# Optimization experiments

Hardware: AMD Instinct MI355X
Metric: run time of the kernel (lower is better)

## Reference

```python
import jax, jax.numpy as jnp
import numpy as np

LRELU_SLOPE = 0.1  # correlate_operator uses F.leaky_relu_(corr, 0.1)


def _conv2d(x, w, b):
    # x: [B,Ci,H,W], w: [Co,Ci,kh,kw], stride 1, padding SAME (=padding=1 for 3x3)
    y = jax.lax.conv_general_dilated(x, w, (1, 1), 'SAME',
                                     dimension_numbers=('NCHW', 'OIHW', 'NCHW'))
    return y + b[None, :, None, None]


def correlate(x1, x2):
    # spatial_correlation_sample(x1, x2, kernel_size=3, patch_size=1, stride=1,
    # padding=1): with patch_size=1 the only displacement is (0,0), so the cost
    # volume is a 3x3 window sum of the per-pixel channel dot product.
    # Then divided by C and leaky_relu(0.1) as in correlate_operator.
    prod = jnp.sum(x1 * x2, axis=1, keepdims=True)  # [B,1,H,W]
    box = jnp.ones((1, 1, 3, 3), prod.dtype)
    corr = jax.lax.conv_general_dilated(prod, box, (1, 1), 'SAME',
                                        dimension_numbers=('NCHW', 'OIHW', 'NCHW'))
    corr = corr / x1.shape[1]
    return jnp.where(corr > 0, corr, LRELU_SLOPE * corr)


def deform_conv2d(x, offset, w):
    # mmcv DeformConv2d: kernel 3x3, stride 1, pad 1, dilation 1, deform_groups=1,
    # bias=False. offset: [B, 2*kh*kw, H, W], per kernel tap k: (dy_k, dx_k).
    B, Cin, H, W = x.shape
    O, _, kh, kw = w.shape
    K = kh * kw
    off = offset.reshape(B, K, 2, H, W)
    dy, dx = off[:, :, 0], off[:, :, 1]  # [B,K,H,W]
    ky, kx = jnp.meshgrid(jnp.arange(kh), jnp.arange(kw), indexing='ij')
    # sampling position: p + p_k + offset_k (pad=1 cancels the kernel-center shift)
    y = jnp.arange(H, dtype=x.dtype)[None, None, :, None] \
        + (ky.reshape(-1) - kh // 2).astype(x.dtype)[None, :, None, None] + dy
    xx = jnp.arange(W, dtype=x.dtype)[None, None, None, :] \
        + (kx.reshape(-1) - kw // 2).astype(x.dtype)[None, :, None, None] + dx
    y0 = jnp.floor(y)
    x0 = jnp.floor(xx)
    wy = (y - y0)[:, None]   # [B,1,K,H,W]
    wx = (xx - x0)[:, None]
    y0i = y0.astype(jnp.int32)
    x0i = x0.astype(jnp.int32)
    xf = x.reshape(B, Cin, H * W)

    def gather(yi, xi):
        valid = (yi >= 0) & (yi < H) & (xi >= 0) & (xi < W)  # zero padding outside
        idx = jnp.clip(yi, 0, H - 1) * W + jnp.clip(xi, 0, W - 1)
        v = jnp.take_along_axis(xf, idx.reshape(B, 1, K * H * W), axis=2)
        return v.reshape(B, Cin, K, H, W) * valid.astype(x.dtype)[:, None]

    v00 = gather(y0i, x0i)
    v01 = gather(y0i, x0i + 1)
    v10 = gather(y0i + 1, x0i)
    v11 = gather(y0i + 1, x0i + 1)
    samp = (v00 * (1 - wy) * (1 - wx) + v01 * (1 - wy) * wx
            + v10 * wy * (1 - wx) + v11 * wy * wx)  # [B,Cin,K,H,W]
    return jnp.einsum('bckhw,ock->bohw', samp, w.reshape(O, Cin, K))


def setup_inputs() -> dict:
    key = jax.random.key(0)
    ks = jax.random.split(key, 10)
    B, C, H, W = 4, 256, 64, 64
    s = 0.02
    return {
        'x_ref': jax.random.normal(ks[0], (B, C, H, W), jnp.float32),
        'x_next': jax.random.normal(ks[1], (B, C, H, W), jnp.float32),
        'w1': jax.random.normal(ks[2], (256, 1, 3, 3), jnp.float32) * s,
        'b1': jax.random.normal(ks[3], (256,), jnp.float32) * s,
        'w2': jax.random.normal(ks[4], (256, 256, 3, 3), jnp.float32) * s,
        'b2': jax.random.normal(ks[5], (256,), jnp.float32) * s,
        'w3': jax.random.normal(ks[6], (18, 256, 3, 3), jnp.float32) * s,
        'b3': jax.random.normal(ks[7], (18,), jnp.float32) * s,
        'w_dcn': jax.random.normal(ks[8], (256, 256, 3, 3), jnp.float32) * s,
        'idx': 4,
    }


def reference(x_ref, x_next, w1, b1, w2, b2, w3, b3, w_dcn, idx):
    # idx=4 -> corr_patch_size=1 (consistent with conv1 in_channels)
    corr = correlate(x_next, x_ref)                      # [B,1,H,W]
    h = jax.nn.relu(_conv2d(corr, w1, b1))               # [B,256,H,W]
    h = jax.nn.relu(_conv2d(h, w2, b2))                  # [B,256,H,W]
    offset = jax.nn.relu(_conv2d(h, w3, b3))             # [B,18,H,W]
    x_ref_cal = jax.nn.relu(deform_conv2d(x_ref, offset, w_dcn))
    return 0.5 * (x_next + x_ref_cal)
```

## Files before the change

### kernel.cpp

```cpp
#include <hip/hip_runtime.h>

typedef __attribute__((ext_vector_type(8))) short short8v;
typedef __attribute__((ext_vector_type(4))) float f32x4;
typedef __attribute__((ext_vector_type(2))) float f32x2;
typedef __attribute__((ext_vector_type(4))) unsigned int u32x4;

constexpr int Bsz = 4;
constexpr int Hh = 64, Wwd = 64;
constexpr int HWp = Hh * Wwd;
constexpr int NPIX = Bsz * HWp;
constexpr int HH = 66;
constexpr int HPIX = HH * HH;
constexpr int Kdim = 2304;
constexpr int NSTEP = 36;

constexpr size_t B_H1H  = 0;
constexpr size_t HALO_BYTES = (size_t)Bsz * HPIX * 256 * 2;
constexpr size_t B_H2H  = B_H1H + HALO_BYTES;
constexpr size_t B_XTH  = B_H2H + HALO_BYTES;
constexpr size_t B_PROD = B_XTH + HALO_BYTES;
constexpr size_t B_OFFP = B_PROD + (size_t)NPIX * 4;
constexpr size_t B_WB2  = B_OFFP + (size_t)NPIX * 32 * 4;
constexpr size_t B_WBD  = B_WB2 + (size_t)256 * Kdim * 2;
constexpr size_t B_WB3  = B_WBD + (size_t)256 * Kdim * 2;

static __device__ __forceinline__ unsigned short f2bf(float f) {
    unsigned u = __builtin_bit_cast(unsigned, f);
    u += 0x7FFFu + ((u >> 16) & 1u);
    return (unsigned short)(u >> 16);
}
static __device__ __forceinline__ unsigned cvt_pk_bf16(float lo, float hi) {
    unsigned r;
    asm("v_cvt_pk_bf16_f32 %0, %1, %2" : "=v"(r) : "v"(lo), "v"(hi));
    return r;
}
static __device__ __forceinline__ f32x2 pk_mul(f32x2 a, f32x2 b) {
    f32x2 d;
    asm("v_pk_mul_f32 %0, %1, %2" : "=v"(d) : "v"(a), "v"(b));
    return d;
}
static __device__ __forceinline__ f32x2 pk_fma(f32x2 a, f32x2 b, f32x2 c) {
    f32x2 d;
    asm("v_pk_fma_f32 %0, %1, %2, %3" : "=v"(d) : "v"(a), "v"(b), "v"(c));
    return d;
}
static __device__ __forceinline__ f32x2 unpack2(unsigned u) {
    f32x2 v;
    v.x = __builtin_bit_cast(float, u << 16);
    v.y = __builtin_bit_cast(float, u & 0xFFFF0000u);
    return v;
}
static __device__ __forceinline__ void gload_lds16(const void* g, void* l) {
    __builtin_amdgcn_global_load_lds((const __attribute__((address_space(1))) unsigned int*)g,
                                     (__attribute__((address_space(3))) unsigned int*)l, 16, 0, 0);
}
static __device__ __forceinline__ int swz(int u) {
    return (((u & 7) ^ ((u >> 3) & 7)) << 3);
}

__global__ void k_zero_ring(unsigned short* h1h, unsigned short* h2h, unsigned short* xth,
                            float* prod) {
    int blk = blockIdx.x;
    if (blk >= 3120) {
        unsigned* p = (unsigned*)prod + (size_t)(blk - 3120) * 128 + threadIdx.x;
        *p = 0;
        return;
    }
    int img = blk / 260;
    int rp = blk - img * 260;
    int buf = img >> 2, b = img & 3;
    int y, x;
    if (rp < 66) { y = 0; x = rp; }
    else if (rp < 132) { y = 65; x = rp - 66; }
    else { int s2 = rp - 132; y = 1 + (s2 >> 1); x = (s2 & 1) * 65; }
    unsigned short* base = (buf == 0) ? h1h : (buf == 1) ? h2h : xth;
    unsigned* p = (unsigned*)(base + ((size_t)b * HPIX + y * HH + x) * 256);
    p[threadIdx.x] = 0;
}

__global__ void k_prodx(const float* __restrict__ xr, const float* __restrict__ xn,
                        unsigned short* __restrict__ xth, float* __restrict__ prod) {
    __shared__ float t[32][33];
    __shared__ float red[8][33];
    int b = blockIdx.z;
    int c0 = blockIdx.y * 32;
    int y = blockIdx.x >> 1, x0 = (blockIdx.x & 1) * 32;
    int tx = threadIdx.x, ty = threadIdx.y;
    float part = 0.f;
#pragma unroll
    for (int i = 0; i < 32; i += 8) {
        size_t idx = ((size_t)b * 256 + c0 + ty + i) * HWp + y * Wwd + x0 + tx;
        float vr = xr[idx];
        float vn = xn[idx];
        t[ty + i][tx] = vr;
        part = fmaf(vr, vn, part);
    }
    red[ty][tx] = part;
    __syncthreads();
#pragma unroll
    for (int i = 0; i < 32; i += 8)
        xth[((size_t)b * HPIX + (y + 1) * HH + (x0 + ty + i + 1)) * 256 + c0 + tx] =
            f2bf(t[tx][ty + i]);
    if (ty == 0) {
        float s = red[0][tx] + red[1][tx] + red[2][tx] + red[3][tx] +
                  red[4][tx] + red[5][tx] + red[6][tx] + red[7][tx];
        atomicAdd(&prod[b * HWp + y * Wwd + x0 + tx], s);
    }
}

__global__ __launch_bounds__(256) void k_conv1c(const float* __restrict__ prod,
                                                const float* __restrict__ w1,
                                                const float* __restrict__ b1,
                                                unsigned short* __restrict__ h1h) {
    __shared__ float pp[5][36];
    __shared__ float pt[3][34];
    int px0 = blockIdx.x * 32;
    int b = px0 >> 12, y = (px0 & 4095) >> 6, x0 = px0 & 63;
    int tid = threadIdx.x;
    if (tid < 180) {
        int i = tid / 36, j = tid - i * 36;
        int yy = y - 2 + i, xx = x0 - 2 + j;
        float v = 0.f;
        if (yy >= 0 && yy < Hh && xx >= 0 && xx < Wwd) v = prod[b * HWp + yy * Wwd + xx];
        pp[i][j] = v;
    }
    __syncthreads();
    if (tid < 102) {
        int i = tid / 34, j = tid - i * 34;
        int yy = y - 1 + i, xx = x0 - 1 + j;
        float v = 0.f;
        if (yy >= 0 && yy < Hh && xx >= 0 && xx < Wwd) {
            float s = pp[i][j]     + pp[i][j + 1]     + pp[i][j + 2] +
                      pp[i + 1][j] + pp[i + 1][j + 1] + pp[i + 1][j + 2] +
                      pp[i + 2][j] + pp[i + 2][j + 1] + pp[i + 2][j + 2];
            s *= (1.0f / 256.0f);
            v = (s > 0.f) ? s : 0.1f * s;
        }
        pt[i][j] = v;
    }
    float wl[9];
#pragma unroll
    for (int k = 0; k < 9; ++k) wl[k] = w1[tid * 9 + k];
    float bias = b1[tid];
    __syncthreads();
    for (int p = 0; p < 32; ++p) {
        float acc = bias;
#pragma unroll
        for (int ky = 0; ky < 3; ++ky)
#pragma unroll
            for (int kx = 0; kx < 3; ++kx) acc = fmaf(pt[ky][p + kx], wl[ky * 3 + kx], acc);
        acc = fmaxf(acc, 0.f);
        h1h[((size_t)b * HPIX + (y + 1) * HH + (x0 + p + 1)) * 256 + tid] = f2bf(acc);
    }
}

__global__ void k_packall(const float* __restrict__ w2, const float* __restrict__ wd,
                          const float* __restrict__ w3,
                          unsigned short* __restrict__ wb2f, unsigned short* __restrict__ wbdf,
                          unsigned short* __restrict__ wb3) {
    int blk = blockIdx.x;
    if (blk < 4608) {
        const float* w = (blk < 2304) ? w2 : wd;
        unsigned short* out = (blk < 2304) ? wb2f : wbdf;
        int i = (blk % 2304) * 256 + threadIdx.x;
        int e = i & 7;
        int lane = (i >> 3) & 63;
        int mi = (i >> 9) & 1;
        int kf = (i >> 10) & 1;
        int rest = i >> 11;
        int s = rest % 36;
        int wv = rest / 36;
        int o = wv * 32 + mi * 16 + (lane & 15);
        int kk = s * 64 + (kf * 4 + (lane >> 4)) * 8 + e;
        int c = kk & 255, tap = kk >> 8;
        out[i] = f2bf(w[((size_t)o * 256 + c) * 9 + tap]);
    } else {
        int i = (blk - 4608) * 256 + threadIdx.x;
        int o = i / Kdim;
        int r = i - o * Kdim;
        int k = r >> 8, c = r & 255;
        float v = (o < 18) ? w3[((size_t)o * 256 + c) * 9 + k] : 0.f;
        wb3[i] = f2bf(v);
    }
}

__global__ __launch_bounds__(256) void k_conv2g(const unsigned short* __restrict__ h1h,
                                                const unsigned short* __restrict__ wbf,
                                                const float* __restrict__ bias,
                                                unsigned short* __restrict__ h2h) {
    __shared__ short S_s[4][64 * 64];
    const int tid = threadIdx.x;
    const int bid = blockIdx.x;
    const int lin = (bid & 7) * 64 + (bid >> 3);
    const int px0 = (lin >> 1) * 64;
    const int oblk = lin & 1;
    const int b = px0 >> 12;
    const unsigned short* hb = h1h + (size_t)b * HPIX * 256;
    const int pxl = tid >> 2;
    const int px = px0 + pxl;
    const int y = (px & 4095) >> 6, x = px & 63;
    const int u0 = (tid & 3) * 2;
    const int lane = tid & 63, wv = tid >> 6;
    const int ot = oblk * 4 + wv;
    const unsigned short* wfb = wbf + (size_t)ot * NSTEP * 2048 + lane * 8;
    const unsigned short* abase0 = hb + (size_t)((y + 1) * HH + (x + 1)) * 256 + u0 * 8;

    f32x4 acc[4][2] = {};
    u32x4 wA[2][4], wB[2][4];
    u32x4 aP[4], aQ[4];
    float bia[2];
#pragma unroll
    for (int oi = 0; oi < 2; ++oi) bia[oi] = bias[ot * 32 + oi * 16 + (lane & 15)];

    const int wr0 = pxl * 64 + ((u0 ^ (pxl & 7)) << 3);
    const int wr1 = pxl * 64 + (((u0 + 1) ^ (pxl & 7)) << 3);

    auto WLOAD = [&](int s, u32x4 (&wreg)[4]) {
#pragma unroll
        for (int f = 0; f < 4; ++f)
            wreg[f] = *(const u32x4*)(wfb + ((size_t)s * 4 + f) * 512);
    };
    auto ALOAD = [&](int s, u32x4& a0, u32x4& a1) {
        int tap = s >> 2, chunk = s & 3;
        int aoff = ((tap / 3 - 1) * HH + (tap % 3 - 1)) * 256 + chunk * 64;
        a0 = *(const u32x4*)(abase0 + aoff);
        a1 = *(const u32x4*)(abase0 + aoff + 8);
    };

    {
        u32x4 a0, a1, a2, a3;
        ALOAD(0, a0, a1);
        ALOAD(1, a2, a3);
        WLOAD(0, wA[0]);
        WLOAD(1, wA[1]);
        *(u32x4*)&S_s[0][wr0] = a0;
        *(u32x4*)&S_s[0][wr1] = a1;
        *(u32x4*)&S_s[1][wr0] = a2;
        *(u32x4*)&S_s[1][wr1] = a3;
        ALOAD(2, aP[0], aP[1]);
        ALOAD(3, aP[2], aP[3]);
        asm volatile("s_waitcnt lgkmcnt(0)" ::: "memory");
    }

    auto ITER2 = [&](int s, u32x4 (&wcur)[2][4], u32x4 (&wnxt)[2][4],
                     u32x4 (&aC)[4], u32x4 (&aN)[4], short* SBc, short* SBn) {
        __builtin_amdgcn_s_barrier();
        __builtin_amdgcn_sched_barrier(0);
        if (s + 2 < NSTEP) {
            *(u32x4*)&SBn[wr0] = aC[0];
            *(u32x4*)&SBn[wr1] = aC[1];
            *(u32x4*)&SBn[64 * 64 + wr0] = aC[2];
            *(u32x4*)&SBn[64 * 64 + wr1] = aC[3];
        }
        if (s + 4 < NSTEP) {
            ALOAD(s + 4, aN[0], aN[1]);
            ALOAD(s + 5, aN[2], aN[3]);
        }
        if (s + 2 < NSTEP) {
            WLOAD(s + 2, wnxt[0]);
            WLOAD(s + 3, wnxt[1]);
        }
#pragma unroll
        for (int half = 0; half < 2; ++half) {
            const short* SB = SBc + half * 64 * 64;
            short8v af[4][2];
#pragma unroll
            for (int pi = 0; pi < 4; ++pi) {
                int row = pi * 16 + (lane & 15);
#pragma unroll
                for (int kf = 0; kf < 2; ++kf) {
                    int c8 = kf * 4 + (lane >> 4);
                    af[pi][kf] = *(const short8v*)&SB[row * 64 + ((c8 ^ (row & 7)) << 3)];
                }
            }
            __builtin_amdgcn_s_setprio(1);
#pragma unroll
            for (int kf = 0; kf < 2; ++kf)
#pragma unroll
                for (int pi = 0; pi < 4; ++pi)
#pragma unroll
                    for (int oi = 0; oi < 2; ++oi)
                        acc[pi][oi] = __builtin_amdgcn_mfma_f32_16x16x32_bf16(
                            af[pi][kf], __builtin_bit_cast(short8v, wcur[half][kf * 2 + oi]),
                            acc[pi][oi], 0, 0, 0);
            __builtin_amdgcn_s_setprio(0);
        }
        asm volatile("s_waitcnt lgkmcnt(0)" ::: "memory");
    };

    for (int s4 = 0; s4 < NSTEP; s4 += 4) {
        ITER2(s4, wA, wB, aP, aQ, &S_s[0][0], &S_s[2][0]);
        ITER2(s4 + 2, wB, wA, aQ, aP, &S_s[2][0], &S_s[0][0]);
    }

#pragma unroll
    for (int pi = 0; pi < 4; ++pi) {
#pragma unroll
        for (int j = 0; j < 4; ++j) {
            int p2 = px0 + pi * 16 + (lane >> 4) * 4 + j;
            int yy = (p2 & 4095) >> 6, xx = p2 & 63;
            unsigned short* dst = h2h + ((size_t)b * HPIX + (yy + 1) * HH + (xx + 1)) * 256;
#pragma unroll
            for (int oi = 0; oi < 2; ++oi) {
                int o = ot * 32 + oi * 16 + (lane & 15);
                dst[o] = f2bf(fmaxf(acc[pi][oi][j] + bia[oi], 0.f));
            }
        }
    }
}

__global__ __launch_bounds__(256) void k_conv3g(const unsigned short* __restrict__ h2h,
                                                const unsigned short* __restrict__ wb,
                                                const float* __restrict__ bias,
                                                float* __restrict__ offp) {
    __shared__ short A_s[2][64 * 64];
    __shared__ short B_s[2][32 * 64];
    const int tid = threadIdx.x;
    const int px0 = blockIdx.x * 64;
    const int b = px0 >> 12;
    const unsigned short* hb = h2h + (size_t)b * HPIX * 256;

    const unsigned short* abase[2];
#pragma unroll
    for (int i = 0; i < 2; ++i) {
        int u = i * 256 + tid;
        int pxl = u >> 3;
        int pxg = px0 + pxl;
        int y = (pxg & 4095) >> 6, x = pxg & 63;
        abase[i] = hb + (size_t)((y + 1) * HH + (x + 1)) * 256 + swz(u);
    }
    const unsigned short* bbase = wb + (size_t)(tid >> 3) * Kdim + swz(tid);

    const int lane = tid & 63, wv = tid >> 6;
    f32x4 acc[2] = {};

    auto STAGE = [&](int s, int buf) {
        int tap = s >> 2, chunk = s & 3;
        int delta = ((tap / 3 - 1) * HH + (tap % 3 - 1)) * 256 + chunk * 64;
        short* Ab = &A_s[buf][0];
#pragma unroll
        for (int i = 0; i < 2; ++i) gload_lds16(abase[i] + delta, Ab + (i * 256 + tid) * 8);
        gload_lds16(bbase + s * 64, &B_s[buf][tid * 8]);
    };

    STAGE(0, 0);
    __syncthreads();
    for (int s = 0; s < NSTEP; ++s) {
        int cur = s & 1;
        if (s + 1 < NSTEP) STAGE(s + 1, cur ^ 1);
        const short* Ab = &A_s[cur][0];
        const short* Bb = &B_s[cur][0];
        short8v af[2], bf[2][2];
#pragma unroll
        for (int kf = 0; kf < 2; ++kf) {
            int row = wv * 16 + (lane & 15);
            int c8 = kf * 4 + (lane >> 4);
            af[kf] = *(const short8v*)&Ab[row * 64 + ((c8 ^ (row & 7)) << 3)];
        }
#pragma unroll
        for (int ni = 0; ni < 2; ++ni) {
            int row = ni * 16 + (lane & 15);
#pragma unroll
            for (int kf = 0; kf < 2; ++kf) {
                int c8 = kf * 4 + (lane >> 4);
                bf[ni][kf] = *(const short8v*)&B_s[cur][row * 64 + ((c8 ^ (row & 7)) << 3)];
            }
        }
#pragma unroll
        for (int kf = 0; kf < 2; ++kf)
#pragma unroll
            for (int ni = 0; ni < 2; ++ni)
                acc[ni] = __builtin_amdgcn_mfma_f32_16x16x32_bf16(af[kf], bf[ni][kf], acc[ni], 0, 0, 0);
        __syncthreads();
    }
#pragma unroll
    for (int j = 0; j < 4; ++j) {
        int px = px0 + wv * 16 + (lane >> 4) * 4 + j;
#pragma unroll
        for (int ni = 0; ni < 2; ++ni) {
            int o = ni * 16 + (lane & 15);
            float bv = (o < 18) ? bias[o] : 0.f;
            offp[(size_t)px * 32 + o] = fmaxf(acc[ni][j] + bv, 0.f);
        }
    }
}

__global__ __launch_bounds__(512) void k_dcng(const unsigned short* __restrict__ xth,
                                              const float* __restrict__ offp,
                                              const unsigned short* __restrict__ wbf,
                                              const float* __restrict__ xn,
                                              float* __restrict__ out) {
    __shared__ short S_s[4][64 * 64];
    const int tid = threadIdx.x;
    const int bid = blockIdx.x;
    const int px0 = ((bid & 7) * 32 + (bid >> 3)) * 64;
    const int b = px0 >> 12;
    const unsigned short* xb = xth + (size_t)b * HPIX * 256;
    const int pxl = tid >> 3;
    const int px = px0 + pxl;
    const int y = (px & 4095) >> 6, x = px & 63;
    const int u0 = tid & 7;
    const int lane = tid & 63, wv = tid >> 6;
    const unsigned short* wfb = wbf + (size_t)wv * NSTEP * 2048 + lane * 8;
    const float2* offv = (const float2*)offp;

    f32x4 acc[2][4] = {};
    u32x4 wA[2][4], wB[2][4];
    u32x4 g[2][4];
    const int wr0 = pxl * 64 + ((u0 ^ (pxl & 7)) << 3);

    const unsigned short* pcorner[4];
    f32x2 wpair[4];
    float2 offn;

    auto SETUP = [&](int tap, float dyo, float dxo) {
        int ky = tap / 3 - 1, kx = tap % 3 - 1;
        float ypos = (float)(y + ky) + dyo;
        float xpos = (float)(x + kx) + dxo;
        float y0f = floorf(ypos), x0f = floorf(xpos);
        float wy = ypos - y0f, wx = xpos - x0f;
        int y0 = (int)y0f, x0 = (int)x0f;
        bool y0v = (y0 >= 0) && (y0 < Hh), y1v = (y0 + 1 >= 0) && (y0 + 1 < Hh);
        bool x0v = (x0 >= 0) && (x0 < Wwd), x1v = (x0 + 1 >= 0) && (x0 + 1 < Wwd);
        int hy0 = min(max(y0, -1), 64) + 1, hy1 = min(max(y0 + 1, -1), 64) + 1;
        int hx0 = min(max(x0, -1), 64) + 1, hx1 = min(max(x0 + 1, -1), 64) + 1;
        float w0 = (1.f - wy) * (1.f - wx) * (float)(y0v && x0v);
        float w1 = (1.f - wy) * wx * (float)(y0v && x1v);
        float w2 = wy * (1.f - wx) * (float)(y1v && x0v);
        float w3 = wy * wx * (float)(y1v && x1v);
        wpair[0] = (f32x2){w0, w0};
        wpair[1] = (f32x2){w1, w1};
        wpair[2] = (f32x2){w2, w2};
        wpair[3] = (f32x2){w3, w3};
        pcorner[0] = xb + (size_t)((hy0 * HH + hx0) * 256) + u0 * 8;
        pcorner[1] = xb + (size_t)((hy0 * HH + hx1) * 256) + u0 * 8;
        pcorner[2] = xb + (size_t)((hy1 * HH + hx0) * 256) + u0 * 8;
        pcorner[3] = xb + (size_t)((hy1 * HH + hx1) * 256) + u0 * 8;
    };
    auto WLOAD = [&](int s, u32x4 (&wreg)[4]) {
#pragma unroll
        for (int f = 0; f < 4; ++f)
            wreg[f] = *(const u32x4*)(wfb + ((size_t)s * 4 + f) * 512);
    };
    auto GISSUE = [&](int s, u32x4 (&gr)[4]) {
        const int nco = (s & 3) * 64;
#pragma unroll
        for (int c = 0; c < 4; ++c) gr[c] = *(const u32x4*)(pcorner[c] + nco);
    };
    auto COMBINE_WRITE = [&](u32x4 (&gr)[4], short* SBn) {
        u32x4 res;
#pragma unroll
        for (int qd = 0; qd < 4; ++qd) {
            f32x2 a = pk_mul(unpack2(gr[0][qd]), wpair[0]);
            a = pk_fma(unpack2(gr[1][qd]), wpair[1], a);
            a = pk_fma(unpack2(gr[2][qd]), wpair[2], a);
            a = pk_fma(unpack2(gr[3][qd]), wpair[3], a);
            res[qd] = cvt_pk_bf16(a.x, a.y);
        }
        *(u32x4*)&SBn[wr0] = res;
    };

    {
        float2 o0 = offv[(size_t)px * 16];
        SETUP(0, o0.x, o0.y);
        u32x4 g0[4], g1[4];
        GISSUE(0, g0);
        GISSUE(1, g1);
        WLOAD(0, wA[0]);
        WLOAD(1, wA[1]);
        COMBINE_WRITE(g0, &S_s[0][0]);
        COMBINE_WRITE(g1, &S_s[1][0]);
        GISSUE(2, g[0]);
        GISSUE(3, g[1]);
        offn = offv[(size_t)px * 16 + 1];
        asm volatile("s_waitcnt lgkmcnt(0)" ::: "memory");
    }

    auto ITER2 = [&](int s, u32x4 (&wcur)[2][4], u32x4 (&wnxt)[2][4], short* SBc, short* SBn) {
        __builtin_amdgcn_s_barrier();
        __builtin_amdgcn_sched_barrier(0);
        if (s + 2 < NSTEP) {
            COMBINE_WRITE(g[0], SBn);
            COMBINE_WRITE(g[1], SBn + 64 * 64);
        }
        if ((s & 3) == 0 && s + 4 < NSTEP)
            SETUP((s + 4) >> 2, offn.x, offn.y);
        if ((s & 3) == 2 && ((s + 8) >> 2) < 9)
            offn = offv[(size_t)px * 16 + ((s + 8) >> 2)];
        if (s + 4 < NSTEP) {
            GISSUE(s + 4, g[0]);
            GISSUE(s + 5, g[1]);
        }
        if (s + 2 < NSTEP) {
            WLOAD(s + 2, wnxt[0]);
            WLOAD(s + 3, wnxt[1]);
        }
#pragma unroll
        for (int half = 0; half < 2; ++half) {
            const short* SB = SBc + half * 64 * 64;
            short8v sf[4][2];
#pragma unroll
            for (int ni = 0; ni < 4; ++ni) {
                int row = ni * 16 + (lane & 15);
#pragma unroll
                for (int kf = 0; kf < 2; ++kf) {
                    int c8 = kf * 4 + (lane >> 4);
                    sf[ni][kf] = *(const short8v*)&SB[row * 64 + ((c8 ^ (row & 7)) << 3)];
                }
            }
            __builtin_amdgcn_s_setprio(1);
#pragma unroll
            for (int kf = 0; kf < 2; ++kf)
#pragma unroll
                for (int mi = 0; mi < 2; ++mi)
#pragma unroll
                    for (int ni = 0; ni < 4; ++ni)
                        acc[mi][ni] = __builtin_amdgcn_mfma_f32_16x16x32_bf16(
                            __builtin_bit_cast(short8v, wcur[half][kf * 2 + mi]), sf[ni][kf],
                            acc[mi][ni], 0, 0, 0);
            __builtin_amdgcn_s_setprio(0);
        }
        asm volatile("s_waitcnt lgkmcnt(0)" ::: "memory");
    };

    for (int s4 = 0; s4 < NSTEP; s4 += 4) {
        ITER2(s4, wA, wB, &S_s[0][0], &S_s[2][0]);
        ITER2(s4 + 2, wB, wA, &S_s[2][0], &S_s[0][0]);
    }

#pragma unroll
    for (int mi = 0; mi < 2; ++mi) {
        int o = wv * 32 + mi * 16 + (lane >> 4) * 4;
#pragma unroll
        for (int j = 0; j < 4; ++j) {
            size_t rowbase = ((size_t)b * 256 + o + j) * HWp;
#pragma unroll
            for (int ni = 0; ni < 4; ++ni) {
                int p2 = (px0 + ni * 16 + (lane & 15)) & 4095;
                size_t idx = rowbase + p2;
                out[idx] = 0.5f * (xn[idx] + fmaxf(acc[mi][ni][j], 0.f));
            }
        }
    }
}

extern "C" void kernel_launch(void* const* d_in, const int* in_sizes, int n_in,
                              void* d_out, int out_size, void* d_ws, size_t ws_size,
                              hipStream_t stream) {
    const float* x_ref  = (const float*)d_in[0];
    const float* x_next = (const float*)d_in[1];
    const float* w1 = (const float*)d_in[2];
    const float* b1 = (const float*)d_in[3];
    const float* w2 = (const float*)d_in[4];
    const float* b2 = (const float*)d_in[5];
    const float* w3 = (const float*)d_in[6];
    const float* b3 = (const float*)d_in[7];
    const float* wd = (const float*)d_in[8];
    float* out = (float*)d_out;
    char* ws = (char*)d_ws;

    unsigned short* h1h = (unsigned short*)(ws + B_H1H);
    unsigned short* h2h = (unsigned short*)(ws + B_H2H);
    unsigned short* xth = (unsigned short*)(ws + B_XTH);
    float* prod = (float*)(ws + B_PROD);
    float* offp = (float*)(ws + B_OFFP);
    unsigned short* wb2f = (unsigned short*)(ws + B_WB2);
    unsigned short* wbdf = (unsigned short*)(ws + B_WBD);
    unsigned short* wb3  = (unsigned short*)(ws + B_WB3);

    k_zero_ring<<<3120 + 128, 128, 0, stream>>>(h1h, h2h, xth, prod);
    k_prodx<<<dim3(128, 8, Bsz), dim3(32, 8), 0, stream>>>(x_ref, x_next, xth, prod);
    k_packall<<<4896, 256, 0, stream>>>(w2, wd, w3, wb2f, wbdf, wb3);
    k_conv1c<<<NPIX / 32, 256, 0, stream>>>(prod, w1, b1, h1h);
    k_conv2g<<<512, 256, 0, stream>>>(h1h, wb2f, b2, h2h);
    k_conv3g<<<256, 256, 0, stream>>>(h2h, wb3, b3, offp);
    k_dcng<<<256, 512, 0, stream>>>(xth, offp, wbdf, x_next, out);
}
```

Measured before the change: 107.5 us.

## Restructure conv3 GEMM with register-held prepacked weights and deeper pipelining

The conv3 (256->18 offset) kernel stops staging A and B through global_load_lds. It now loads activations into registers, writes them to a swizzled 4-buffer LDS ring two steps ahead, and reads weights straight into registers from a new MFMA-fragment-packed layout produced by k_packall. Blocks are remapped across images in the same way as conv2/dcn, and the loop is unrolled two steps per barrier with setprio around the MFMAs. The aim is to hide load latency and cut LDS traffic and barriers, at the cost of more registers and more complex scheduling.

```diff
diff --git a/kernel.cpp b/kernel.cpp
--- a/kernel.cpp
+++ b/kernel.cpp
@@ -49,10 +49,6 @@
     v.x = __builtin_bit_cast(float, u << 16);
     v.y = __builtin_bit_cast(float, u & 0xFFFF0000u);
     return v;
-}
-static __device__ __forceinline__ void gload_lds16(const void* g, void* l) {
-    __builtin_amdgcn_global_load_lds((const __attribute__((address_space(1))) unsigned int*)g,
-                                     (__attribute__((address_space(3))) unsigned int*)l, 16, 0, 0);
 }
 static __device__ __forceinline__ int swz(int u) {
     return (((u & 7) ^ ((u >> 3) & 7)) << 3);
@@ -157,7 +153,7 @@
 __global__ void k_packall(const float* __restrict__ w2, const float* __restrict__ wd,
                           const float* __restrict__ w3,
                           unsigned short* __restrict__ wb2f, unsigned short* __restrict__ wbdf,
-                          unsigned short* __restrict__ wb3) {
+                          unsigned short* __restrict__ wb3f) {
     int blk = blockIdx.x;
     if (blk < 4608) {
         const float* w = (blk < 2304) ? w2 : wd;
@@ -176,11 +172,16 @@
         out[i] = f2bf(w[((size_t)o * 256 + c) * 9 + tap]);
     } else {
         int i = (blk - 4608) * 256 + threadIdx.x;
-        int o = i / Kdim;
-        int r = i - o * Kdim;
-        int k = r >> 8, c = r & 255;
-        float v = (o < 18) ? w3[((size_t)o * 256 + c) * 9 + k] : 0.f;
-        wb3[i] = f2bf(v);
+        int e = i & 7;
+        int lane = (i >> 3) & 63;
+        int oi = (i >> 9) & 1;
+        int kf = (i >> 10) & 1;
+        int s = i >> 11;
+        int o = oi * 16 + (lane & 15);
+        int kk = s * 64 + (kf * 4 + (lane >> 4)) * 8 + e;
+        int c = kk & 255, tap = kk >> 8;
+        float v = (o < 18) ? w3[((size_t)o * 256 + c) * 9 + tap] : 0.f;
+        wb3f[i] = f2bf(v);
     }
 }
 
@@ -310,77 +311,116 @@
 }
 
 __global__ __launch_bounds__(256) void k_conv3g(const unsigned short* __restrict__ h2h,
-                                                const unsigned short* __restrict__ wb,
+                                                const unsigned short* __restrict__ wb3f,
                                                 const float* __restrict__ bias,
                                                 float* __restrict__ offp) {
-    __shared__ short A_s[2][64 * 64];
-    __shared__ short B_s[2][32 * 64];
+    __shared__ short S_s[4][64 * 64];
     const int tid = threadIdx.x;
-    const int px0 = blockIdx.x * 64;
+    const int bid = blockIdx.x;
+    const int px0 = ((bid & 7) * 32 + (bid >> 3)) * 64;
     const int b = px0 >> 12;
     const unsigned short* hb = h2h + (size_t)b * HPIX * 256;
-
-    const unsigned short* abase[2];
-#pragma unroll
-    for (int i = 0; i < 2; ++i) {
-        int u = i * 256 + tid;
-        int pxl = u >> 3;
-        int pxg = px0 + pxl;
-        int y = (pxg & 4095) >> 6, x = pxg & 63;
-        abase[i] = hb + (size_t)((y + 1) * HH + (x + 1)) * 256 + swz(u);
-    }
-    const unsigned short* bbase = wb + (size_t)(tid >> 3) * Kdim + swz(tid);
-
+    const int pxl = tid >> 2;
+    const int px = px0 + pxl;
+    const int y = (px & 4095) >> 6, x = px & 63;
+    const int u0 = (tid & 3) * 2;
     const int lane = tid & 63, wv = tid >> 6;
+    const unsigned short* wfb = wb3f + lane * 8;
+    const unsigned short* abase0 = hb + (size_t)((y + 1) * HH + (x + 1)) * 256 + u0 * 8;
+
     f32x4 acc[2] = {};
-
-    auto STAGE = [&](int s, int buf) {
+    u32x4 wA[2][4], wB[2][4];
+    u32x4 aP[4], aQ[4];
+    float bia[2];
+#pragma unroll
+    for (int oi = 0; oi < 2; ++oi) {
+        int o = oi * 16 + (lane & 15);
+        bia[oi] = (o < 18) ? bias[o] : 0.f;
+    }
+
+    const int wr0 = pxl * 64 + ((u0 ^ (pxl & 7)) << 3);
+    const int wr1 = pxl * 64 + (((u0 + 1) ^ (pxl & 7)) << 3);
+
+    auto WLOAD = [&](int s, u32x4 (&wreg)[4]) {
+#pragma unroll
+        for (int f = 0; f < 4; ++f)
+            wreg[f] = *(const u32x4*)(wfb + ((size_t)s * 4 + f) * 512);
+    };
+    auto ALOAD = [&](int s, u32x4& a0, u32x4& a1) {
         int tap = s >> 2, chunk = s & 3;
-        int delta = ((tap / 3 - 1) * HH + (tap % 3 - 1)) * 256 + chunk * 64;
-        short* Ab = &A_s[buf][0];
-#pragma unroll
-        for (int i = 0; i < 2; ++i) gload_lds16(abase[i] + delta, Ab + (i * 256 + tid) * 8);
-        gload_lds16(bbase + s * 64, &B_s[buf][tid * 8]);
-    };
-
-    STAGE(0, 0);
-    __syncthreads();
-    for (int s = 0; s < NSTEP; ++s) {
-        int cur = s & 1;
-        if (s + 1 < NSTEP) STAGE(s + 1, cur ^ 1);
-        const short* Ab = &A_s[cur][0];
-        const short* Bb = &B_s[cur][0];
-        short8v af[2], bf[2][2];
-#pragma unroll
-        for (int kf = 0; kf < 2; ++kf) {
-            int row = wv * 16 + (lane & 15);
-            int c8 = kf * 4 + (lane >> 4);
-            af[kf] = *(const short8v*)&Ab[row * 64 + ((c8 ^ (row & 7)) << 3)];
-        }
-#pragma unroll
-        for (int ni = 0; ni < 2; ++ni) {
-            int row = ni * 16 + (lane & 15);
+        int aoff = ((tap / 3 - 1) * HH + (tap % 3 - 1)) * 256 + chunk * 64;
+        a0 = *(const u32x4*)(abase0 + aoff);
+        a1 = *(const u32x4*)(abase0 + aoff + 8);
+    };
+
+    {
+        u32x4 a0, a1, a2, a3;
+        ALOAD(0, a0, a1);
+        ALOAD(1, a2, a3);
+        WLOAD(0, wA[0]);
+        WLOAD(1, wA[1]);
+        *(u32x4*)&S_s[0][wr0] = a0;
+        *(u32x4*)&S_s[0][wr1] = a1;
+        *(u32x4*)&S_s[1][wr0] = a2;
+        *(u32x4*)&S_s[1][wr1] = a3;
+        ALOAD(2, aP[0], aP[1]);
+        ALOAD(3, aP[2], aP[3]);
+        asm volatile("s_waitcnt lgkmcnt(0)" ::: "memory");
+    }
+
+    auto ITER2 = [&](int s, u32x4 (&wcur)[2][4], u32x4 (&wnxt)[2][4],
+                     u32x4 (&aC)[4], u32x4 (&aN)[4], short* SBc, short* SBn) {
+        __builtin_amdgcn_s_barrier();
+        __builtin_amdgcn_sched_barrier(0);
+        if (s + 2 < NSTEP) {
+            *(u32x4*)&SBn[wr0] = aC[0];
+            *(u32x4*)&SBn[wr1] = aC[1];
+            *(u32x4*)&SBn[64 * 64 + wr0] = aC[2];
+            *(u32x4*)&SBn[64 * 64 + wr1] = aC[3];
+        }
+        if (s + 4 < NSTEP) {
+            ALOAD(s + 4, aN[0], aN[1]);
+            ALOAD(s + 5, aN[2], aN[3]);
+        }
+        if (s + 2 < NSTEP) {
+            WLOAD(s + 2, wnxt[0]);
+            WLOAD(s + 3, wnxt[1]);
+        }
+#pragma unroll
+        for (int half = 0; half < 2; ++half) {
+            const short* SB = SBc + half * 64 * 64;
+            short8v af[2];
 #pragma unroll
             for (int kf = 0; kf < 2; ++kf) {
+                int row = wv * 16 + (lane & 15);
                 int c8 = kf * 4 + (lane >> 4);
-                bf[ni][kf] = *(const short8v*)&B_s[cur][row * 64 + ((c8 ^ (row & 7)) << 3)];
+                af[kf] = *(const short8v*)&SB[row * 64 + ((c8 ^ (row & 7)) << 3)];
             }
-        }
-#pragma unroll
-        for (int kf = 0; kf < 2; ++kf)
-#pragma unroll
-            for (int ni = 0; ni < 2; ++ni)
-                acc[ni] = __builtin_amdgcn_mfma_f32_16x16x32_bf16(af[kf], bf[ni][kf], acc[ni], 0, 0, 0);
-        __syncthreads();
-    }
+            __builtin_amdgcn_s_setprio(1);
+#pragma unroll
+            for (int kf = 0; kf < 2; ++kf)
+#pragma unroll
+                for (int oi = 0; oi < 2; ++oi)
+                    acc[oi] = __builtin_amdgcn_mfma_f32_16x16x32_bf16(
+                        af[kf], __builtin_bit_cast(short8v, wcur[half][kf * 2 + oi]),
+                        acc[oi], 0, 0, 0);
+            __builtin_amdgcn_s_setprio(0);
+        }
+        asm volatile("s_waitcnt lgkmcnt(0)" ::: "memory");
+    };
+
+    for (int s4 = 0; s4 < NSTEP; s4 += 4) {
+        ITER2(s4, wA, wB, aP, aQ, &S_s[0][0], &S_s[2][0]);
+        ITER2(s4 + 2, wB, wA, aQ, aP, &S_s[2][0], &S_s[0][0]);
+    }
+
 #pragma unroll
     for (int j = 0; j < 4; ++j) {
-        int px = px0 + wv * 16 + (lane >> 4) * 4 + j;
-#pragma unroll
-        for (int ni = 0; ni < 2; ++ni) {
-            int o = ni * 16 + (lane & 15);
-            float bv = (o < 18) ? bias[o] : 0.f;
-            offp[(size_t)px * 32 + o] = fmaxf(acc[ni][j] + bv, 0.f);
+        int p2 = px0 + wv * 16 + (lane >> 4) * 4 + j;
+#pragma unroll
+        for (int oi = 0; oi < 2; ++oi) {
+            int o = oi * 16 + (lane & 15);
+            offp[(size_t)p2 * 32 + o] = fmaxf(acc[oi][j] + bia[oi], 0.f);
         }
     }
 }
@@ -566,13 +606,13 @@
     float* offp = (float*)(ws + B_OFFP);
     unsigned short* wb2f = (unsigned short*)(ws + B_WB2);
     unsigned short* wbdf = (unsigned short*)(ws + B_WBD);
-    unsigned short* wb3  = (unsigned short*)(ws + B_WB3);
+    unsigned short* wb3f = (unsigned short*)(ws + B_WB3);
 
     k_zero_ring<<<3120 + 128, 128, 0, stream>>>(h1h, h2h, xth, prod);
     k_prodx<<<dim3(128, 8, Bsz), dim3(32, 8), 0, stream>>>(x_ref, x_next, xth, prod);
-    k_packall<<<4896, 256, 0, stream>>>(w2, wd, w3, wb2f, wbdf, wb3);
+    k_packall<<<4896, 256, 0, stream>>>(w2, wd, w3, wb2f, wbdf, wb3f);
     k_conv1c<<<NPIX / 32, 256, 0, stream>>>(prod, w1, b1, h1h);
     k_conv2g<<<512, 256, 0, stream>>>(h1h, wb2f, b2, h2h);
-    k_conv3g<<<256, 256, 0, stream>>>(h2h, wb3, b3, offp);
+    k_conv3g<<<256, 256, 0, stream>>>(h2h, wb3f, b3, offp);
     k_dcng<<<256, 512, 0, stream>>>(xth, offp, wbdf, x_next, out);
 }
```

Result: faster. 97.49 us (-9.3%).
